# Performance work log

Measured on AMD Instinct MI355X. Metric: run time of the kernel, lower is better.

Reference implementation:

```python
import jax, jax.numpy as jnp
import numpy as np

N_DENSE = 13
N_FIELDS = 26
FEAT_NUM_PER_FIELD = 100000
FEATURE_NUM = N_FIELDS * FEAT_NUM_PER_FIELD + N_DENSE  # 2_600_013
K = 16
BATCH = 4096


def setup_inputs() -> dict:
    key = jax.random.key(0)
    k1, k2, k3, k4 = jax.random.split(key, 4)
    dense_inputs = jax.random.normal(k1, (BATCH, N_DENSE), dtype=jnp.float32)
    sparse_inputs = jax.random.randint(k2, (BATCH, N_FIELDS), 0, FEAT_NUM_PER_FIELD, dtype=jnp.int32)
    # learned params (tf.random_normal_initializer default stddev=0.05)
    w0 = jnp.zeros((1,), dtype=jnp.float32)
    w = 0.05 * jax.random.normal(k3, (FEATURE_NUM, 1), dtype=jnp.float32)
    V = 0.05 * jax.random.normal(k4, (K, FEATURE_NUM), dtype=jnp.float32)
    return {"dense_inputs": dense_inputs, "sparse_inputs": sparse_inputs,
            "w0": w0, "w": w, "V": V}


def reference(dense_inputs, sparse_inputs, w0, w, V):
    # Equivalent to: stack = concat([dense, one_hot(sparse_fields)], axis=1)
    # followed by FM first/second order terms, expressed as gathers
    # (one_hot @ M == M[offset + idx]; one_hot**2 == one_hot).
    n_dense = dense_inputs.shape[1]          # 13
    n_fields = sparse_inputs.shape[1]        # 26
    per_field = (w.shape[0] - n_dense) // n_fields
    offsets = n_dense + jnp.arange(n_fields, dtype=sparse_inputs.dtype) * per_field
    idx = sparse_inputs + offsets[None, :]   # [B, 26] global row indices

    # first order: w0 + stack @ w
    first = w0 + dense_inputs @ w[:n_dense] \
            + jnp.sum(w[idx, 0], axis=1, keepdims=True)  # [B, 1]

    Vt = V.T                                  # [feature_num, k]
    g = Vt[idx]                               # [B, 26, k] gathered latent vecs
    # e = stack @ V.T ; sq = stack**2 @ (V.T)**2 (one-hot entries square to themselves)
    e = dense_inputs @ Vt[:n_dense] + jnp.sum(g, axis=1)                  # [B, k]
    sq = (dense_inputs ** 2) @ (Vt[:n_dense] ** 2) + jnp.sum(g ** 2, axis=1)
    second = 0.5 * jnp.sum(e ** 2 - sq, axis=1, keepdims=True)            # [B, 1]

    return first + second
```

## Files before the change

### kernel.cpp

```cpp
#include <hip/hip_runtime.h>

#define N_DENSE 13
#define N_FIELDS 26
#define PER_FIELD 100000
#define FEATURE_NUM (N_FIELDS * PER_FIELD + N_DENSE)
#define K_DIM 16
#define BATCH 4096

__global__ __launch_bounds__(256) void fm_layer_kernel(
    const float* __restrict__ dense,
    const int*   __restrict__ sparse,
    const float* __restrict__ w0,
    const float* __restrict__ w,
    const float* __restrict__ V,
    float*       __restrict__ out)
{
    const int wave_in_block = threadIdx.x >> 6;
    const int lane = threadIdx.x & 63;
    const int b = blockIdx.x * (blockDim.x >> 6) + wave_in_block;
    if (b >= BATCH) return;

    const int k    = lane & 15;
    const int fsub = lane >> 4;

    const size_t vrow = (size_t)k * FEATURE_NUM;

    int gidx[7];
    #pragma unroll
    for (int i = 0; i < 7; ++i) {
        int f = fsub + 4 * i;
        if (f < N_FIELDS) {
            gidx[i] = N_DENSE + f * PER_FIELD + sparse[b * N_FIELDS + f];
        } else {
            gidx[i] = -1;
        }
    }

    float e = 0.f, sq = 0.f, lin = 0.f;

    #pragma unroll
    for (int d = fsub; d < N_DENSE; d += 4) {
        float x = dense[b * N_DENSE + d];
        float v = V[vrow + d];
        e  += x * v;
        sq += (x * x) * (v * v);
        if (k == 0) lin += x * w[d];
    }

    #pragma unroll
    for (int i = 0; i < 7; ++i) {
        if (gidx[i] >= 0) {
            size_t g = (size_t)gidx[i];
            float v = V[vrow + g];
            e  += v;
            sq += v * v;
            if (k == 0) lin += w[g];
        }
    }

    e  += __shfl_xor(e, 16, 64);
    e  += __shfl_xor(e, 32, 64);
    sq += __shfl_xor(sq, 16, 64);
    sq += __shfl_xor(sq, 32, 64);

    float t = e * e - sq;

    #pragma unroll
    for (int m = 1; m <= 8; m <<= 1) {
        t   += __shfl_xor(t, m, 64);
        lin += __shfl_xor(lin, m, 64);
    }
    lin += __shfl_xor(lin, 16, 64);
    lin += __shfl_xor(lin, 32, 64);

    if (lane == 0) {
        out[b] = w0[0] + lin + 0.5f * t;
    }
}

extern "C" void kernel_launch(void* const* d_in, const int* in_sizes, int n_in,
                              void* d_out, int out_size, void* d_ws, size_t ws_size,
                              hipStream_t stream) {
    const float* dense  = (const float*)d_in[0];
    const int*   sparse = (const int*)d_in[1];
    const float* w0     = (const float*)d_in[2];
    const float* w      = (const float*)d_in[3];
    const float* V      = (const float*)d_in[4];
    float* out = (float*)d_out;

    const int waves_per_block = 4;
    const int blocks = BATCH / waves_per_block;
    fm_layer_kernel<<<blocks, 256, 0, stream>>>(dense, sparse, w0, w, V, out);
}
```

Baseline: 241.0 us.

## Transpose V to row-major in workspace, then gather contiguous float4 rows

Adds a pre-pass that transposes V into a feature-major layout in the workspace, so each gathered latent vector is one contiguous 64-byte row read as float4s. The gather kernel is restructured so that each lane loads one float4 of one field, with two waves per batch row combining their results through shared memory. This replaces 16 strided scattered loads per field with one contiguous row load. The cost is a full streaming read and write of the whole V table on every call.

```diff
diff --git a/kernel.cpp b/kernel.cpp
--- a/kernel.cpp
+++ b/kernel.cpp
@@ -7,74 +7,103 @@
 #define K_DIM 16
 #define BATCH 4096
 
-__global__ __launch_bounds__(256) void fm_layer_kernel(
+__global__ __launch_bounds__(256) void transpose_v_kernel(
+    const float* __restrict__ V,
+    float*       __restrict__ Vt)
+{
+    const int stride = gridDim.x * blockDim.x;
+    for (int f = blockIdx.x * blockDim.x + threadIdx.x; f < FEATURE_NUM; f += stride) {
+        float vals[K_DIM];
+        #pragma unroll
+        for (int k = 0; k < K_DIM; ++k) {
+            vals[k] = V[(size_t)k * FEATURE_NUM + f];
+        }
+        float4* dst = (float4*)(Vt + (size_t)f * K_DIM);
+        #pragma unroll
+        for (int j = 0; j < 4; ++j) {
+            dst[j] = make_float4(vals[4 * j], vals[4 * j + 1], vals[4 * j + 2], vals[4 * j + 3]);
+        }
+    }
+}
+
+__global__ __launch_bounds__(256) void fm_gather_kernel(
     const float* __restrict__ dense,
     const int*   __restrict__ sparse,
     const float* __restrict__ w0,
     const float* __restrict__ w,
-    const float* __restrict__ V,
+    const float* __restrict__ Vt,
     float*       __restrict__ out)
 {
-    const int wave_in_block = threadIdx.x >> 6;
-    const int lane = threadIdx.x & 63;
-    const int b = blockIdx.x * (blockDim.x >> 6) + wave_in_block;
-    if (b >= BATCH) return;
+    const int wave  = threadIdx.x >> 6;
+    const int lane  = threadIdx.x & 63;
+    const int row   = wave >> 1;
+    const int halfw = wave & 1;
+    const int b = blockIdx.x * 2 + row;
 
-    const int k    = lane & 15;
-    const int fsub = lane >> 4;
+    const int fL = lane >> 2;
+    const int q  = lane & 3;
+    const int f  = halfw * 16 + fL;
 
-    const size_t vrow = (size_t)k * FEATURE_NUM;
+    const float4* Vt4 = (const float4*)Vt;
 
-    int gidx[7];
-    #pragma unroll
-    for (int i = 0; i < 7; ++i) {
-        int f = fsub + 4 * i;
-        if (f < N_FIELDS) {
-            gidx[i] = N_DENSE + f * PER_FIELD + sparse[b * N_FIELDS + f];
-        } else {
-            gidx[i] = -1;
-        }
+    float e[4]  = {0.f, 0.f, 0.f, 0.f};
+    float sq[4] = {0.f, 0.f, 0.f, 0.f};
+    float lin = 0.f;
+
+    if (f < N_FIELDS) {
+        const int g = N_DENSE + f * PER_FIELD + sparse[b * N_FIELDS + f];
+        float4 v = Vt4[(size_t)g * 4 + q];
+        e[0] += v.x; e[1] += v.y; e[2] += v.z; e[3] += v.w;
+        sq[0] += v.x * v.x; sq[1] += v.y * v.y; sq[2] += v.z * v.z; sq[3] += v.w * v.w;
+        if (q == 0) lin += w[g];
     }
 
-    float e = 0.f, sq = 0.f, lin = 0.f;
-
-    #pragma unroll
-    for (int d = fsub; d < N_DENSE; d += 4) {
-        float x = dense[b * N_DENSE + d];
-        float v = V[vrow + d];
-        e  += x * v;
-        sq += (x * x) * (v * v);
-        if (k == 0) lin += x * w[d];
+    if (halfw == 0 && f < N_DENSE) {
+        const float x = dense[b * N_DENSE + f];
+        float4 v = Vt4[(size_t)f * 4 + q];
+        e[0] += x * v.x; e[1] += x * v.y; e[2] += x * v.z; e[3] += x * v.w;
+        const float x2 = x * x;
+        sq[0] += x2 * v.x * v.x; sq[1] += x2 * v.y * v.y;
+        sq[2] += x2 * v.z * v.z; sq[3] += x2 * v.w * v.w;
+        if (q == 0) lin += x * w[f];
     }
 
     #pragma unroll
-    for (int i = 0; i < 7; ++i) {
-        if (gidx[i] >= 0) {
-            size_t g = (size_t)gidx[i];
-            float v = V[vrow + g];
-            e  += v;
-            sq += v * v;
-            if (k == 0) lin += w[g];
+    for (int m = 4; m <= 32; m <<= 1) {
+        #pragma unroll
+        for (int c = 0; c < 4; ++c) {
+            e[c]  += __shfl_xor(e[c], m, 64);
+            sq[c] += __shfl_xor(sq[c], m, 64);
+        }
+        lin += __shfl_xor(lin, m, 64);
+    }
+
+    __shared__ float sE[2][2][4][4];
+    __shared__ float sS[2][2][4][4];
+    __shared__ float sL[2][2];
+    if (lane < 4) {
+        #pragma unroll
+        for (int c = 0; c < 4; ++c) {
+            sE[row][halfw][q][c] = e[c];
+            sS[row][halfw][q][c] = sq[c];
         }
     }
+    if (lane == 0) sL[row][halfw] = lin;
+    __syncthreads();
 
-    e  += __shfl_xor(e, 16, 64);
-    e  += __shfl_xor(e, 32, 64);
-    sq += __shfl_xor(sq, 16, 64);
-    sq += __shfl_xor(sq, 32, 64);
-
-    float t = e * e - sq;
-
-    #pragma unroll
-    for (int m = 1; m <= 8; m <<= 1) {
-        t   += __shfl_xor(t, m, 64);
-        lin += __shfl_xor(lin, m, 64);
-    }
-    lin += __shfl_xor(lin, 16, 64);
-    lin += __shfl_xor(lin, 32, 64);
-
-    if (lane == 0) {
-        out[b] = w0[0] + lin + 0.5f * t;
+    if (halfw == 0 && lane < 4) {
+        float t = 0.f;
+        #pragma unroll
+        for (int c = 0; c < 4; ++c) {
+            float eT = sE[row][0][q][c] + sE[row][1][q][c];
+            float sT = sS[row][0][q][c] + sS[row][1][q][c];
+            t += eT * eT - sT;
+        }
+        t += __shfl_xor(t, 1, 64);
+        t += __shfl_xor(t, 2, 64);
+        if (lane == 0) {
+            out[b] = w0[0] + sL[row][0] + sL[row][1] + 0.5f * t;
+        }
     }
 }
 
@@ -87,8 +116,8 @@
     const float* w      = (const float*)d_in[3];
     const float* V      = (const float*)d_in[4];
     float* out = (float*)d_out;
+    float* Vt  = (float*)d_ws;
 
-    const int waves_per_block = 4;
-    const int blocks = BATCH / waves_per_block;
-    fm_layer_kernel<<<blocks, 256, 0, stream>>>(dense, sparse, w0, w, V, out);
+    transpose_v_kernel<<<2048, 256, 0, stream>>>(V, Vt);
+    fm_gather_kernel<<<BATCH / 2, 256, 0, stream>>>(dense, sparse, w0, w, Vt, out);
 }
```

Result: slower. 296.2 us (+22.9%).

## Split FM into transpose, field-major gather, and reduction kernels

Applied to the files above, without the earlier changes.

Replaces the single per-row kernel with three kernels. The first transposes the sparse indices. The second gathers V and w values with one block per (field, k) pair and writes them to a workspace. The third reduces over fields and latent dimensions with coalesced reads. Grouping every gather for one field and latent row into the same block should let the random lookups share cache lines in L2 instead of scattering across the whole table. In exchange it writes and re-reads a workspace of roughly 7 MB and adds two extra kernel launches.

```diff
diff --git a/kernel.cpp b/kernel.cpp
--- a/kernel.cpp
+++ b/kernel.cpp
@@ -7,74 +7,100 @@
 #define K_DIM 16
 #define BATCH 4096
 
-__global__ __launch_bounds__(256) void fm_layer_kernel(
+#define WS_V_OFF   0
+#define WS_L_OFF   (N_FIELDS * K_DIM * BATCH)
+#define WS_S_OFF   (WS_L_OFF + N_FIELDS * BATCH)
+
+__global__ __launch_bounds__(256) void transpose_sparse_kernel(
+    const int* __restrict__ sparse, int* __restrict__ sT)
+{
+    const int b = blockIdx.x * blockDim.x + threadIdx.x;
+    if (b >= BATCH) return;
+    #pragma unroll
+    for (int f = 0; f < N_FIELDS; ++f) {
+        sT[f * BATCH + b] = sparse[b * N_FIELDS + f];
+    }
+}
+
+__global__ __launch_bounds__(512) void gather_kernel(
+    const int*   __restrict__ sT,
+    const float* __restrict__ w,
+    const float* __restrict__ V,
+    float*       __restrict__ ws_v,
+    float*       __restrict__ ws_lin)
+{
+    const int f = blockIdx.x >> 4;
+    const int k = blockIdx.x & 15;
+    const int tid = threadIdx.x;
+
+    const int base = N_DENSE + f * PER_FIELD;
+    const float* __restrict__ Vrow = V + (size_t)k * FEATURE_NUM + base;
+    const int* __restrict__ sTf = sT + f * BATCH;
+
+    int   idx[8];
+    float v[8];
+    #pragma unroll
+    for (int r = 0; r < 8; ++r) idx[r] = sTf[r * 512 + tid];
+    #pragma unroll
+    for (int r = 0; r < 8; ++r) v[r] = Vrow[idx[r]];
+    float* __restrict__ dst = ws_v + ((size_t)f * K_DIM + k) * BATCH;
+    #pragma unroll
+    for (int r = 0; r < 8; ++r) dst[r * 512 + tid] = v[r];
+
+    if (k == 0) {
+        const float* __restrict__ wf = w + base;
+        float wl[8];
+        #pragma unroll
+        for (int r = 0; r < 8; ++r) wl[r] = wf[idx[r]];
+        float* __restrict__ dl = ws_lin + (size_t)f * BATCH;
+        #pragma unroll
+        for (int r = 0; r < 8; ++r) dl[r * 512 + tid] = wl[r];
+    }
+}
+
+__global__ __launch_bounds__(256) void reduce_kernel(
     const float* __restrict__ dense,
-    const int*   __restrict__ sparse,
     const float* __restrict__ w0,
     const float* __restrict__ w,
     const float* __restrict__ V,
+    const float* __restrict__ ws_v,
+    const float* __restrict__ ws_lin,
     float*       __restrict__ out)
 {
-    const int wave_in_block = threadIdx.x >> 6;
-    const int lane = threadIdx.x & 63;
-    const int b = blockIdx.x * (blockDim.x >> 6) + wave_in_block;
-    if (b >= BATCH) return;
+    const int bl = threadIdx.x & 15;
+    const int k  = threadIdx.x >> 4;
+    const int b  = blockIdx.x * 16 + bl;
 
-    const int k    = lane & 15;
-    const int fsub = lane >> 4;
-
-    const size_t vrow = (size_t)k * FEATURE_NUM;
-
-    int gidx[7];
+    float e = 0.f, sq = 0.f;
     #pragma unroll
-    for (int i = 0; i < 7; ++i) {
-        int f = fsub + 4 * i;
-        if (f < N_FIELDS) {
-            gidx[i] = N_DENSE + f * PER_FIELD + sparse[b * N_FIELDS + f];
-        } else {
-            gidx[i] = -1;
-        }
+    for (int f = 0; f < N_FIELDS; ++f) {
+        float v = ws_v[((size_t)f * K_DIM + k) * BATCH + b];
+        e  += v;
+        sq += v * v;
     }
-
-    float e = 0.f, sq = 0.f, lin = 0.f;
-
     #pragma unroll
-    for (int d = fsub; d < N_DENSE; d += 4) {
-        float x = dense[b * N_DENSE + d];
-        float v = V[vrow + d];
-        e  += x * v;
-        sq += (x * x) * (v * v);
-        if (k == 0) lin += x * w[d];
+    for (int d = 0; d < N_DENSE; ++d) {
+        float x  = dense[b * N_DENSE + d];
+        float vv = V[(size_t)k * FEATURE_NUM + d];
+        e  += x * vv;
+        sq += (x * x) * (vv * vv);
     }
-
-    #pragma unroll
-    for (int i = 0; i < 7; ++i) {
-        if (gidx[i] >= 0) {
-            size_t g = (size_t)gidx[i];
-            float v = V[vrow + g];
-            e  += v;
-            sq += v * v;
-            if (k == 0) lin += w[g];
-        }
-    }
-
-    e  += __shfl_xor(e, 16, 64);
-    e  += __shfl_xor(e, 32, 64);
-    sq += __shfl_xor(sq, 16, 64);
-    sq += __shfl_xor(sq, 32, 64);
-
     float t = e * e - sq;
 
-    #pragma unroll
-    for (int m = 1; m <= 8; m <<= 1) {
-        t   += __shfl_xor(t, m, 64);
-        lin += __shfl_xor(lin, m, 64);
-    }
-    lin += __shfl_xor(lin, 16, 64);
-    lin += __shfl_xor(lin, 32, 64);
+    __shared__ float sTile[K_DIM][17];
+    sTile[k][bl] = t;
+    __syncthreads();
 
-    if (lane == 0) {
-        out[b] = w0[0] + lin + 0.5f * t;
+    if (k == 0) {
+        float tt = 0.f;
+        #pragma unroll
+        for (int kk = 0; kk < K_DIM; ++kk) tt += sTile[kk][bl];
+        float lin = 0.f;
+        #pragma unroll
+        for (int f = 0; f < N_FIELDS; ++f) lin += ws_lin[f * BATCH + b];
+        #pragma unroll
+        for (int d = 0; d < N_DENSE; ++d) lin += dense[b * N_DENSE + d] * w[d];
+        out[b] = w0[0] + lin + 0.5f * tt;
     }
 }
 
@@ -88,7 +114,12 @@
     const float* V      = (const float*)d_in[4];
     float* out = (float*)d_out;
 
-    const int waves_per_block = 4;
-    const int blocks = BATCH / waves_per_block;
-    fm_layer_kernel<<<blocks, 256, 0, stream>>>(dense, sparse, w0, w, V, out);
+    float* wsf    = (float*)d_ws;
+    float* ws_v   = wsf + WS_V_OFF;
+    float* ws_lin = wsf + WS_L_OFF;
+    int*   sT     = (int*)(wsf + WS_S_OFF);
+
+    transpose_sparse_kernel<<<BATCH / 256, 256, 0, stream>>>(sparse, sT);
+    gather_kernel<<<N_FIELDS * K_DIM, 512, 0, stream>>>(sT, w, V, ws_v, ws_lin);
+    reduce_kernel<<<BATCH / 16, 256, 0, stream>>>(dense, w0, w, V, ws_v, ws_lin, out);
 }
```

New measurement: 263.9 us. 1.1x slower.
